# Optimization experiments

Measured on AMD Instinct MI355X. Metric: run time of the kernel, lower is better.

## Reference

```python
import jax, jax.numpy as jnp
import numpy as np

TAU = 0.5
LOGIT_TAU = float(np.log(TAU / (1.0 - TAU)))  # = 0.0 for tau=0.5
N_STEPS = 128           # torch samples randint(128,129) -> always 128
N_SECANT = 8
D_MIN, D_MAX = 0.0, 2.4
B, N, HID, CDIM = 4, 8192, 64, 128


def decoder(p, c, W1, Wc, b1, W2, b2):
    """Occupancy-logit MLP. p: (B, ..., 3), c: (B, CDIM) -> (B, ...)."""
    cc = c @ Wc  # (B, HID)
    cc = cc.reshape(cc.shape[:1] + (1,) * (p.ndim - 2) + cc.shape[1:])
    h = jax.nn.relu(jnp.einsum('...d,dh->...h', p, W1) + cc + b1)
    return (h @ W2 + b2)[..., 0]


def setup_inputs() -> dict:
    key = jax.random.key(0)
    ks = jax.random.split(key, 8)
    return {
        'ray0': jax.random.normal(ks[0], (B, N, 3), jnp.float32) * 0.5,
        'ray_direction': jax.random.normal(ks[1], (B, N, 3), jnp.float32),
        'c': jax.random.normal(ks[2], (B, CDIM), jnp.float32),
        'W1': jax.random.normal(ks[3], (3, HID), jnp.float32) * 0.5,
        'Wc': jax.random.normal(ks[4], (CDIM, HID), jnp.float32) * 0.1,
        'b1': jax.random.normal(ks[5], (HID,), jnp.float32) * 0.1,
        'W2': jax.random.normal(ks[6], (HID, 1), jnp.float32) * 0.5,
        'b2': jax.random.normal(ks[7], (1,), jnp.float32) * 0.1,
    }


def reference(ray0, ray_direction, c, W1, Wc, b1, W2, b2):
    S = N_STEPS
    bsz, npts, _ = ray0.shape
    dec = lambda p: decoder(p, c, W1, Wc, b1, W2, b2)

    # --- coarse ray marching ---
    d_prop = jnp.linspace(D_MIN, D_MAX, S).astype(ray0.dtype)        # (S,)
    p_prop = ray0[:, :, None, :] + ray_direction[:, :, None, :] * d_prop[None, None, :, None]
    val = dec(p_prop) - LOGIT_TAU                                    # (B, N, S)

    mask_0_not_occupied = val[:, :, 0] < 0
    sign_matrix = jnp.concatenate(
        [jnp.sign(val[:, :, :-1] * val[:, :, 1:]),
         jnp.ones((bsz, npts, 1), val.dtype)], axis=-1)
    cost_matrix = sign_matrix * jnp.arange(S, 0, -1, dtype=val.dtype)
    indices = jnp.argmin(cost_matrix, axis=-1)                       # (B, N)
    values = jnp.min(cost_matrix, axis=-1)
    mask_sign_change = values < 0
    f_low = jnp.take_along_axis(val, indices[..., None], axis=2)[..., 0]
    mask_neg_to_pos = f_low < 0
    mask = mask_sign_change & mask_neg_to_pos & mask_0_not_occupied

    d_prop_full = jnp.broadcast_to(d_prop, (bsz, npts, S))
    d_low = jnp.take_along_axis(d_prop_full, indices[..., None], axis=2)[..., 0]
    idx_hi = jnp.minimum(indices + 1, S - 1)
    d_high = jnp.take_along_axis(d_prop_full, idx_hi[..., None], axis=2)[..., 0]
    f_high = jnp.take_along_axis(val, idx_hi[..., None], axis=2)[..., 0]

    # safe placeholders for non-surface rays (results discarded by mask)
    d_low = jnp.where(mask, d_low, 0.0)
    d_high = jnp.where(mask, d_high, 1.0)
    f_low = jnp.where(mask, f_low, -1.0)
    f_high = jnp.where(mask, f_high, 1.0)

    # --- secant refinement (vectorized over all rays) ---
    d_pred = -f_low * (d_high - d_low) / (f_high - f_low) + d_low
    for _ in range(N_SECANT):
        p_mid = ray0 + d_pred[..., None] * ray_direction
        f_mid = dec(p_mid) - LOGIT_TAU
        ind_low = f_mid < 0
        d_low = jnp.where(ind_low, d_pred, d_low)
        f_low = jnp.where(ind_low, f_mid, f_low)
        d_high = jnp.where(ind_low, d_high, d_pred)
        f_high = jnp.where(ind_low, f_high, f_mid)
        d_pred = -f_low * (d_high - d_low) / (f_high - f_low) + d_low

    d_out = jnp.where(mask, d_pred, jnp.inf)
    d_out = jnp.where(mask_0_not_occupied, d_out, 0.0)
    return d_out
```

## Files before the change

kernel.cpp:

```cpp
#include <hip/hip_runtime.h>
#include <hip/hip_bf16.h>

#define HID   64
#define CDIM  128
#define NSTEP 128
#define NRAYS 32768

typedef const __hip_bfloat16* __restrict__ bf16p;

__device__ __forceinline__ float bf2f(__hip_bfloat16 x) { return __bfloat162float(x); }

__global__ void precompute_cc(bf16p c, bf16p Wc, bf16p b1, float* __restrict__ ccb1) {
    int b = blockIdx.x;
    int h = threadIdx.x;
    float acc = bf2f(b1[h]);
    const __hip_bfloat16* crow = c + b * CDIM;
    for (int k = 0; k < CDIM; ++k)
        acc = fmaf(bf2f(crow[k]), bf2f(Wc[k * HID + h]), acc);
    ccb1[b * HID + h] = acc;
}

__global__ __launch_bounds__(256) void raymarch(
    bf16p ray0, bf16p rdir, bf16p W1, bf16p W2, bf16p b2,
    const float* __restrict__ ccb1, __hip_bfloat16* __restrict__ out) {
    __shared__ float4 sW[HID];
    __shared__ float  sCb[HID];

    const int tid  = threadIdx.x;
    const int wave = tid >> 6;
    const int lane = tid & 63;
    const int r    = blockIdx.x * 4 + wave;
    const int batch = blockIdx.x >> 11;

    if (tid < HID) {
        sW[tid] = make_float4(bf2f(W1[tid]), bf2f(W1[HID + tid]),
                              bf2f(W1[2 * HID + tid]), bf2f(W2[tid]));
    } else if (tid < 2 * HID) {
        int j = tid - HID;
        sCb[j] = ccb1[batch * HID + j];
    }
    __syncthreads();

    const float b2v = bf2f(b2[0]);
    const float ox = bf2f(ray0[r * 3 + 0]), oy = bf2f(ray0[r * 3 + 1]), oz = bf2f(ray0[r * 3 + 2]);
    const float dx = bf2f(rdir[r * 3 + 0]), dy = bf2f(rdir[r * 3 + 1]), dz = bf2f(rdir[r * 3 + 2]);

    const float STEPF = 2.4f / 127.0f;
    const float d0 = bf2f(__float2bfloat16(lane * STEPF));
    const float d1 = bf2f(__float2bfloat16((lane + 64) * STEPF));

    const float px0 = fmaf(d0, dx, ox), py0 = fmaf(d0, dy, oy), pz0 = fmaf(d0, dz, oz);
    const float px1 = fmaf(d1, dx, ox), py1 = fmaf(d1, dy, oy), pz1 = fmaf(d1, dz, oz);

    float acc0 = b2v, acc1 = b2v;
#pragma unroll 8
    for (int j = 0; j < HID; ++j) {
        float4 w  = sW[j];
        float  cb = sCb[j];
        float h0 = fmaf(px0, w.x, fmaf(py0, w.y, fmaf(pz0, w.z, cb)));
        float h1 = fmaf(px1, w.x, fmaf(py1, w.y, fmaf(pz1, w.z, cb)));
        h0 = fmaxf(h0, 0.0f);
        h1 = fmaxf(h1, 0.0f);
        acc0 = fmaf(h0, w.w, acc0);
        acc1 = fmaf(h1, w.w, acc1);
    }
    float val0 = acc0, val1 = acc1;

    float v1l0  = __shfl(val1, 0);
    float valn0 = __shfl_down(val0, 1);
    valn0 = (lane == 63) ? v1l0 : valn0;
    float valn1 = __shfl_down(val1, 1);

    float prod0 = val0 * valn0;
    float sgn0  = (prod0 < 0.0f) ? -1.0f : ((prod0 > 0.0f) ? 1.0f : 0.0f);
    float cost0 = sgn0 * (float)(128 - lane);

    float prod1 = val1 * valn1;
    float sgn1  = (prod1 < 0.0f) ? -1.0f : ((prod1 > 0.0f) ? 1.0f : 0.0f);
    float cost1 = (lane == 63) ? 1.0f
                               : sgn1 * (float)(64 - lane);

    float mc; int mi;
    if (cost0 <= cost1) { mc = cost0; mi = lane; }
    else                { mc = cost1; mi = lane + 64; }
    for (int off = 32; off > 0; off >>= 1) {
        float oc = __shfl_xor(mc, off);
        int   oi = __shfl_xor(mi, off);
        if (oc < mc || (oc == mc && oi < mi)) { mc = oc; mi = oi; }
    }

    const int idx  = mi;
    const int idxh = (idx + 1 < NSTEP) ? idx + 1 : NSTEP - 1;

    float va  = __shfl(val0, idx  & 63);
    float vb  = __shfl(val1, idx  & 63);
    float f_low  = (idx  < 64) ? va  : vb;
    float vah = __shfl(val0, idxh & 63);
    float vbh = __shfl(val1, idxh & 63);
    float f_high = (idxh < 64) ? vah : vbh;

    float v00 = __shfl(val0, 0);
    bool  m0   = v00 < 0.0f;
    bool  mask = (mc < 0.0f) && (f_low < 0.0f) && m0;

    float result;
    if (mask) {
        float dl = bf2f(__float2bfloat16(idx  * STEPF));
        float dh = bf2f(__float2bfloat16(idxh * STEPF));
        float fl = f_low, fh = f_high;
        const float4 wl  = sW[lane];
        const float  cbl = sCb[lane];
        float dp = -fl * (dh - dl) / (fh - fl) + dl;
#pragma unroll
        for (int it = 0; it < 8; ++it) {
            float px = fmaf(dp, dx, ox), py = fmaf(dp, dy, oy), pz = fmaf(dp, dz, oz);
            float h = fmaf(px, wl.x, fmaf(py, wl.y, fmaf(pz, wl.z, cbl)));
            h = fmaxf(h, 0.0f);
            float t = h * wl.w;
            for (int off = 32; off > 0; off >>= 1) t += __shfl_xor(t, off);
            float fm = t + b2v;
            bool lowside = fm < 0.0f;
            dl = lowside ? dp : dl;
            fl = lowside ? fm : fl;
            dh = lowside ? dh : dp;
            fh = lowside ? fh : fm;
            dp = -fl * (dh - dl) / (fh - fl) + dl;
        }
        result = dp;
    } else {
        result = m0 ? 0x1.FEp127f : 0.0f;
    }
    if (lane == 0) out[r] = __float2bfloat16(result);
}

extern "C" void kernel_launch(void* const* d_in, const int* in_sizes, int n_in,
                              void* d_out, int out_size, void* d_ws, size_t ws_size,
                              hipStream_t stream) {
    bf16p ray0 = (bf16p)d_in[0];
    bf16p rdir = (bf16p)d_in[1];
    bf16p c    = (bf16p)d_in[2];
    bf16p W1   = (bf16p)d_in[3];
    bf16p Wc   = (bf16p)d_in[4];
    bf16p b1   = (bf16p)d_in[5];
    bf16p W2   = (bf16p)d_in[6];
    bf16p b2   = (bf16p)d_in[7];
    __hip_bfloat16* out = (__hip_bfloat16*)d_out;
    float* ccb1 = (float*)d_ws;

    hipLaunchKernelGGL(precompute_cc, dim3(4), dim3(HID), 0, stream, c, Wc, b1, ccb1);
    hipLaunchKernelGGL(raymarch, dim3(NRAYS / 4), dim3(256), 0, stream,
                       ray0, rdir, W1, W2, b2, ccb1, out);
}
```

Measured before the change: 103.9 us.

## Pack MLP into float2 FMAs, SoA weights, key-packed argmin, split precompute

Result: faster. 100.4 us (-3.4%).

```diff
diff --git a/kernel.cpp b/kernel.cpp
--- a/kernel.cpp
+++ b/kernel.cpp
@@ -7,24 +7,46 @@
 #define NRAYS 32768
 
 typedef const __hip_bfloat16* __restrict__ bf16p;
+typedef float v2f __attribute__((ext_vector_type(2)));
 
 __device__ __forceinline__ float bf2f(__hip_bfloat16 x) { return __bfloat162float(x); }
 
+#if __has_builtin(__builtin_elementwise_fma)
+__device__ __forceinline__ v2f vfma2(v2f a, v2f b, v2f c) { return __builtin_elementwise_fma(a, b, c); }
+#else
+__device__ __forceinline__ v2f vfma2(v2f a, v2f b, v2f c) {
+    v2f r; r.x = fmaf(a.x, b.x, c.x); r.y = fmaf(a.y, b.y, c.y); return r;
+}
+#endif
+#if __has_builtin(__builtin_elementwise_max)
+__device__ __forceinline__ v2f vmax2(v2f a, v2f b) { return __builtin_elementwise_max(a, b); }
+#else
+__device__ __forceinline__ v2f vmax2(v2f a, v2f b) {
+    v2f r; r.x = fmaxf(a.x, b.x); r.y = fmaxf(a.y, b.y); return r;
+}
+#endif
+__device__ __forceinline__ v2f splat2(float s) { v2f v; v.x = s; v.y = s; return v; }
+
 __global__ void precompute_cc(bf16p c, bf16p Wc, bf16p b1, float* __restrict__ ccb1) {
+    __shared__ float part[4][HID];
     int b = blockIdx.x;
-    int h = threadIdx.x;
-    float acc = bf2f(b1[h]);
+    int h = threadIdx.x & 63;
+    int q = threadIdx.x >> 6;
+    float acc = 0.0f;
     const __hip_bfloat16* crow = c + b * CDIM;
-    for (int k = 0; k < CDIM; ++k)
+#pragma unroll
+    for (int k = q * 32; k < q * 32 + 32; ++k)
         acc = fmaf(bf2f(crow[k]), bf2f(Wc[k * HID + h]), acc);
-    ccb1[b * HID + h] = acc;
+    part[q][h] = acc;
+    __syncthreads();
+    if (q == 0)
+        ccb1[b * HID + h] = bf2f(b1[h]) + ((part[0][h] + part[1][h]) + (part[2][h] + part[3][h]));
 }
 
 __global__ __launch_bounds__(256) void raymarch(
     bf16p ray0, bf16p rdir, bf16p W1, bf16p W2, bf16p b2,
     const float* __restrict__ ccb1, __hip_bfloat16* __restrict__ out) {
-    __shared__ float4 sW[HID];
-    __shared__ float  sCb[HID];
+    __shared__ float4 sWX[HID / 4], sWY[HID / 4], sWZ[HID / 4], sW2[HID / 4], sCB[HID / 4];
 
     const int tid  = threadIdx.x;
     const int wave = tid >> 6;
@@ -33,11 +55,11 @@
     const int batch = blockIdx.x >> 11;
 
     if (tid < HID) {
-        sW[tid] = make_float4(bf2f(W1[tid]), bf2f(W1[HID + tid]),
-                              bf2f(W1[2 * HID + tid]), bf2f(W2[tid]));
-    } else if (tid < 2 * HID) {
-        int j = tid - HID;
-        sCb[j] = ccb1[batch * HID + j];
+        ((float*)sWX)[tid] = bf2f(W1[tid]);
+        ((float*)sWY)[tid] = bf2f(W1[HID + tid]);
+        ((float*)sWZ)[tid] = bf2f(W1[2 * HID + tid]);
+        ((float*)sW2)[tid] = bf2f(W2[tid]);
+        ((float*)sCB)[tid] = ccb1[batch * HID + tid];
     }
     __syncthreads();
 
@@ -49,22 +71,31 @@
     const float d0 = bf2f(__float2bfloat16(lane * STEPF));
     const float d1 = bf2f(__float2bfloat16((lane + 64) * STEPF));
 
-    const float px0 = fmaf(d0, dx, ox), py0 = fmaf(d0, dy, oy), pz0 = fmaf(d0, dz, oz);
-    const float px1 = fmaf(d1, dx, ox), py1 = fmaf(d1, dy, oy), pz1 = fmaf(d1, dz, oz);
+    v2f dv; dv.x = d0; dv.y = d1;
+    const v2f pxv = vfma2(dv, splat2(dx), splat2(ox));
+    const v2f pyv = vfma2(dv, splat2(dy), splat2(oy));
+    const v2f pzv = vfma2(dv, splat2(dz), splat2(oz));
 
-    float acc0 = b2v, acc1 = b2v;
-#pragma unroll 8
-    for (int j = 0; j < HID; ++j) {
-        float4 w  = sW[j];
-        float  cb = sCb[j];
-        float h0 = fmaf(px0, w.x, fmaf(py0, w.y, fmaf(pz0, w.z, cb)));
-        float h1 = fmaf(px1, w.x, fmaf(py1, w.y, fmaf(pz1, w.z, cb)));
-        h0 = fmaxf(h0, 0.0f);
-        h1 = fmaxf(h1, 0.0f);
-        acc0 = fmaf(h0, w.w, acc0);
-        acc1 = fmaf(h1, w.w, acc1);
+    v2f acc = splat2(b2v);
+    const v2f zero2 = splat2(0.0f);
+#pragma unroll
+    for (int g = 0; g < HID / 4; ++g) {
+        const float4 wx4 = sWX[g], wy4 = sWY[g], wz4 = sWZ[g], w24 = sW2[g], cb4 = sCB[g];
+        const float* wx = (const float*)&wx4;
+        const float* wy = (const float*)&wy4;
+        const float* wz = (const float*)&wz4;
+        const float* w2 = (const float*)&w24;
+        const float* cb = (const float*)&cb4;
+#pragma unroll
+        for (int jj = 0; jj < 4; ++jj) {
+            v2f h = vfma2(pxv, splat2(wx[jj]),
+                    vfma2(pyv, splat2(wy[jj]),
+                    vfma2(pzv, splat2(wz[jj]), splat2(cb[jj]))));
+            h = vmax2(h, zero2);
+            acc = vfma2(h, splat2(w2[jj]), acc);
+        }
     }
-    float val0 = acc0, val1 = acc1;
+    float val0 = acc.x, val1 = acc.y;
 
     float v1l0  = __shfl(val1, 0);
     float valn0 = __shfl_down(val0, 1);
@@ -80,14 +111,14 @@
     float cost1 = (lane == 63) ? 1.0f
                                : sgn1 * (float)(64 - lane);
 
-    float mc; int mi;
-    if (cost0 <= cost1) { mc = cost0; mi = lane; }
-    else                { mc = cost1; mi = lane + 64; }
-    for (int off = 32; off > 0; off >>= 1) {
-        float oc = __shfl_xor(mc, off);
-        int   oi = __shfl_xor(mi, off);
-        if (oc < mc || (oc == mc && oi < mi)) { mc = oc; mi = oi; }
-    }
+    float key0 = fmaf(cost0, 256.0f, (float)lane);
+    float key1 = fmaf(cost1, 256.0f, (float)(lane + 64));
+    float k = fminf(key0, key1);
+#pragma unroll
+    for (int off = 32; off > 0; off >>= 1)
+        k = fminf(k, __shfl_xor(k, off));
+    const float cf = floorf(k * 0.00390625f);
+    const int   mi = (int)(k - cf * 256.0f);
 
     const int idx  = mi;
     const int idxh = (idx + 1 < NSTEP) ? idx + 1 : NSTEP - 1;
@@ -101,22 +132,25 @@
 
     float v00 = __shfl(val0, 0);
     bool  m0   = v00 < 0.0f;
-    bool  mask = (mc < 0.0f) && (f_low < 0.0f) && m0;
+    bool  mask = (cf < 0.0f) && (f_low < 0.0f) && m0;
 
     float result;
     if (mask) {
         float dl = bf2f(__float2bfloat16(idx  * STEPF));
         float dh = bf2f(__float2bfloat16(idxh * STEPF));
         float fl = f_low, fh = f_high;
-        const float4 wl  = sW[lane];
-        const float  cbl = sCb[lane];
+        const float wlx = ((const float*)sWX)[lane];
+        const float wly = ((const float*)sWY)[lane];
+        const float wlz = ((const float*)sWZ)[lane];
+        const float wl2 = ((const float*)sW2)[lane];
+        const float cbl = ((const float*)sCB)[lane];
         float dp = -fl * (dh - dl) / (fh - fl) + dl;
 #pragma unroll
         for (int it = 0; it < 8; ++it) {
             float px = fmaf(dp, dx, ox), py = fmaf(dp, dy, oy), pz = fmaf(dp, dz, oz);
-            float h = fmaf(px, wl.x, fmaf(py, wl.y, fmaf(pz, wl.z, cbl)));
+            float h = fmaf(px, wlx, fmaf(py, wly, fmaf(pz, wlz, cbl)));
             h = fmaxf(h, 0.0f);
-            float t = h * wl.w;
+            float t = h * wl2;
             for (int off = 32; off > 0; off >>= 1) t += __shfl_xor(t, off);
             float fm = t + b2v;
             bool lowside = fm < 0.0f;
@@ -147,7 +181,7 @@
     __hip_bfloat16* out = (__hip_bfloat16*)d_out;
     float* ccb1 = (float*)d_ws;
 
-    hipLaunchKernelGGL(precompute_cc, dim3(4), dim3(HID), 0, stream, c, Wc, b1, ccb1);
+    hipLaunchKernelGGL(precompute_cc, dim3(4), dim3(256), 0, stream, c, Wc, b1, ccb1);
     hipLaunchKernelGGL(raymarch, dim3(NRAYS / 4), dim3(256), 0, stream,
                        ray0, rdir, W1, W2, b2, ccb1, out);
 }
```
